# Performance work log

Hardware: AMD Instinct MI355X
Metric: run time of the kernel (lower is better)

Reference implementation:

```python
import jax, jax.numpy as jnp
import numpy as np

B, S, F, V, E, H = 128, 256, 4, 1024, 512, 1024
SCALE = 0.05


def setup_inputs() -> dict:
    key = jax.random.key(0)
    ks = jax.random.split(key, 8)
    return {
        "x": jax.random.randint(ks[0], (B, S, F), 0, V),
        "emb": jax.random.normal(ks[1], (F, V, E), dtype=jnp.float32) * SCALE,
        "proj_w": jax.random.normal(ks[2], (E, E), dtype=jnp.float32) * SCALE,
        "proj_b": jnp.zeros((E,), dtype=jnp.float32),
        "W_ih0": jax.random.normal(ks[3], (4 * H, E), dtype=jnp.float32) * SCALE,
        "W_hh0": jax.random.normal(ks[4], (4 * H, H), dtype=jnp.float32) * SCALE,
        "b_ih0": jnp.zeros((4 * H,), dtype=jnp.float32),
        "b_hh0": jnp.zeros((4 * H,), dtype=jnp.float32),
        "W_ih1": jax.random.normal(ks[5], (4 * H, H), dtype=jnp.float32) * SCALE,
        "W_hh1": jax.random.normal(ks[6], (4 * H, H), dtype=jnp.float32) * SCALE,
        "b_ih1": jnp.zeros((4 * H,), dtype=jnp.float32),
        "b_hh1": jnp.zeros((4 * H,), dtype=jnp.float32),
    }


def _lstm_cell(x_t, h, c, W_ih, W_hh, b_ih, b_hh):
    # PyTorch gate layout: [i, f, g, o] along the 4H axis.
    gates = x_t @ W_ih.T + b_ih + h @ W_hh.T + b_hh  # [B, 4H]
    i_pre, f_pre, g_pre, o_pre = jnp.split(gates, 4, axis=-1)
    c_new = jax.nn.sigmoid(f_pre) * c + jax.nn.sigmoid(i_pre) * jnp.tanh(g_pre)
    h_new = jax.nn.sigmoid(o_pre) * jnp.tanh(c_new)
    return h_new, c_new


def reference(x, emb, proj_w, proj_b,
              W_ih0, W_hh0, b_ih0, b_hh0,
              W_ih1, W_hh1, b_ih1, b_hh1):
    # Sum of per-feature embedding lookups: emb[f][x[:, :, f]]  -> [B, S, E]
    emb_sum = jnp.sum(
        jax.vmap(lambda table, idx: table[idx], in_axes=(0, 2))(emb, x), axis=0
    )
    x_in = emb_sum @ proj_w.T + proj_b  # input_proj (Linear)
    xs = jnp.swapaxes(x_in, 0, 1)  # [S, B, E] for scan over time

    z = jnp.zeros((x.shape[0], H), dtype=x_in.dtype)

    def step(carry, x_t):
        h0, c0, h1, c1 = carry
        h0, c0 = _lstm_cell(x_t, h0, c0, W_ih0, W_hh0, b_ih0, b_hh0)
        h1, c1 = _lstm_cell(h0, h1, c1, W_ih1, W_hh1, b_ih1, b_hh1)
        return (h0, c0, h1, c1), h1

    _, h1_seq = jax.lax.scan(step, (z, z, z, z), xs)  # [S, B, H]
    return jnp.swapaxes(h1_seq, 0, 1)  # [B, S, H]
```

## Files before the change

### kernel.cpp

```cpp
#include <hip/hip_runtime.h>
#include <hip/hip_bf16.h>

#define Bb    128
#define Ss    256
#define Ff    4
#define Vv    1024
#define Ee    512
#define Hh    1024
#define FourH 4096
#define Mrows (Bb * Ss)
#define NBLK  192
#define NGRP  8
#define GSZ   (NBLK / NGRP)

typedef _Float16 f16;
typedef __attribute__((ext_vector_type(8))) _Float16 half8;
typedef __attribute__((ext_vector_type(4))) float f32x4;

__global__ void cvt_f16_kernel(const float* __restrict__ s, f16* __restrict__ d, int n) {
    int i = blockIdx.x * blockDim.x + threadIdx.x;
    int stride = gridDim.x * blockDim.x;
    for (; i < n; i += stride) d[i] = (f16)s[i];
}

__global__ void bias_combine_kernel(const float* __restrict__ a, const float* __restrict__ b,
                                    const float* __restrict__ c, const float* __restrict__ d,
                                    float* __restrict__ o0, float* __restrict__ o1) {
    int i = blockIdx.x * blockDim.x + threadIdx.x;
    if (i < FourH) o0[i] = a[i] + b[i];
    else if (i < 2 * FourH) { int j = i - FourH; o1[j] = c[j] + d[j]; }
}

__global__ void emb_kernel(const int* __restrict__ x, const float* __restrict__ emb,
                           f16* __restrict__ out) {
    int r = blockIdx.x;
    int t = threadIdx.x;
    int b = r / Ss, s = r % Ss;
    const int* xr = x + (size_t)r * Ff;
    const float* e0 = emb + (size_t)xr[0] * Ee;
    const float* e1 = emb + (size_t)(Vv + xr[1]) * Ee;
    const float* e2 = emb + (size_t)(2 * Vv + xr[2]) * Ee;
    const float* e3 = emb + (size_t)(3 * Vv + xr[3]) * Ee;
    f16* orow = out + (size_t)(s * Bb + b) * Ee;
    for (int e = t; e < Ee; e += 256) orow[e] = (f16)(e0[e] + e1[e] + e2[e] + e3[e]);
}

#define BM 128
#define BN 128
#define BK 32
#define LDP 40

__global__ __launch_bounds__(256) void gemm_bt_kernel(
    const f16* __restrict__ A, const f16* __restrict__ Bw,
    const float* __restrict__ bias, f16* __restrict__ C,
    int M, int N, int K)
{
    __shared__ f16 As[BM * LDP];
    __shared__ f16 Bs[BN * LDP];
    int tid  = threadIdx.x;
    int n0   = blockIdx.x * BN;
    int m0   = blockIdx.y * BM;
    int w    = tid >> 6, lane = tid & 63;
    int wm   = (w >> 1) * 64, wn = (w & 1) * 64;
    int lrow = lane & 15, koff = lane >> 4;

    f32x4 acc[4][4] = {};

    for (int kb = 0; kb < K; kb += BK) {
        __syncthreads();
        #pragma unroll
        for (int h = 0; h < 2; ++h) {
            int ch  = tid + h * 256;
            int row = ch >> 2;
            int cc  = (ch & 3) * 8;
            *reinterpret_cast<uint4*>(&As[row * LDP + cc]) =
                *reinterpret_cast<const uint4*>(A + (size_t)(m0 + row) * K + kb + cc);
            *reinterpret_cast<uint4*>(&Bs[row * LDP + cc]) =
                *reinterpret_cast<const uint4*>(Bw + (size_t)(n0 + row) * K + kb + cc);
        }
        __syncthreads();
        half8 af[4], bf[4];
        #pragma unroll
        for (int mt = 0; mt < 4; ++mt)
            af[mt] = *reinterpret_cast<const half8*>(&As[(wm + mt * 16 + lrow) * LDP + koff * 8]);
        #pragma unroll
        for (int nt = 0; nt < 4; ++nt)
            bf[nt] = *reinterpret_cast<const half8*>(&Bs[(wn + nt * 16 + lrow) * LDP + koff * 8]);
        #pragma unroll
        for (int mt = 0; mt < 4; ++mt)
            #pragma unroll
            for (int nt = 0; nt < 4; ++nt)
                acc[mt][nt] = __builtin_amdgcn_mfma_f32_16x16x32_f16(af[mt], bf[nt], acc[mt][nt], 0, 0, 0);
    }

    #pragma unroll
    for (int mt = 0; mt < 4; ++mt)
        #pragma unroll
        for (int nt = 0; nt < 4; ++nt) {
            int col = n0 + wn + nt * 16 + lrow;
            float bv = bias[col];
            #pragma unroll
            for (int r = 0; r < 4; ++r) {
                int rowg = m0 + wm + mt * 16 + koff * 4 + r;
                C[(size_t)rowg * N + col] = (f16)(acc[mt][nt][r] + bv);
            }
        }
}

__device__ __forceinline__ void gload_lds16(const void* g, void* l) {
    __builtin_amdgcn_global_load_lds((const __attribute__((address_space(1))) void*)g,
                                     (__attribute__((address_space(3))) void*)l, 16, 0, 0);
}

__device__ __forceinline__ void gst_cc(void* p, unsigned v) {
    asm volatile("global_store_dword %0, %1, off sc0 sc1" :: "v"(p), "v"(v) : "memory");
}

__device__ __forceinline__ float f16lo(unsigned u) {
    return (float)__builtin_bit_cast(f16, (unsigned short)(u & 0xffffu));
}
__device__ __forceinline__ float f16hi(unsigned u) {
    return (float)__builtin_bit_cast(f16, (unsigned short)(u >> 16));
}

__device__ __forceinline__ unsigned aload(unsigned* p) {
    return __hip_atomic_load(p, __ATOMIC_RELAXED, __HIP_MEMORY_SCOPE_AGENT);
}

__device__ __forceinline__ void grid_sync(unsigned* bar, int wg) {
    asm volatile("s_waitcnt vmcnt(0)" ::: "memory");
    __syncthreads();
    if (threadIdx.x == 0) {
        const int g = wg & (NGRP - 1);
        unsigned* arr = bar + g * 32;
        unsigned* rel = bar + (8 + g) * 32;
        unsigned a   = atomicAdd(arr, 1u);
        unsigned gen = a / (unsigned)GSZ;
        if (a % (unsigned)GSZ == (unsigned)(GSZ - 1)) {
            const unsigned tgt = (gen + 1u) * (unsigned)GSZ;
            for (;;) {
                unsigned v0 = aload(bar + 0 * 32), v1 = aload(bar + 1 * 32);
                unsigned v2 = aload(bar + 2 * 32), v3 = aload(bar + 3 * 32);
                unsigned v4 = aload(bar + 4 * 32), v5 = aload(bar + 5 * 32);
                unsigned v6 = aload(bar + 6 * 32), v7 = aload(bar + 7 * 32);
                unsigned mn = min(min(min(v0, v1), min(v2, v3)),
                                  min(min(v4, v5), min(v6, v7)));
                if (mn >= tgt) break;
                __builtin_amdgcn_s_sleep(2);
            }
            atomicAdd(rel, 1u);
        }
        while (aload(rel) < gen + 1u) __builtin_amdgcn_s_sleep(2);
        __builtin_amdgcn_fence(__ATOMIC_ACQUIRE, "agent");
    }
    __syncthreads();
}

__device__ __forceinline__ float sigm(float v) { return 1.f / (1.f + __expf(-v)); }

__global__ __launch_bounds__(512, 2) __attribute__((amdgpu_waves_per_eu(2, 2)))
void scan_kernel(
    const f16* __restrict__ gx0,
    int t_begin, int t_end,
    const f16* __restrict__ wih1, const f16* __restrict__ whh0,
    const f16* __restrict__ whh1, const float* __restrict__ bias1,
    f16* __restrict__ h0a, f16* __restrict__ h0b,
    f16* __restrict__ h1a, f16* __restrict__ h1b,
    float* __restrict__ c0, float* __restrict__ c1,
    float* __restrict__ out, unsigned* __restrict__ bar)
{
    __shared__ __align__(1024) char smem[131072];
    float* ep = (float*)smem;

    const int tid  = threadIdx.x;
    const int wg   = blockIdx.x;
    const int lane = tid & 63;
    const int w    = tid >> 6;
    const int lrow = lane & 15, koff = lane >> 4;
    const unsigned swz   = (unsigned)((lane & 7) << 4);
    const unsigned e0s   = ((unsigned)(koff * 16)) ^ swz;
    const unsigned e1s   = ((unsigned)(64 + koff * 16)) ^ swz;
    const unsigned lane16 = (unsigned)(lane << 4);

    if (wg < 64) {
        const int rowg = wg >> 5, ug = wg & 31;
        const int np = w & 3, kh = w >> 2;
        const int u0 = ug * 32;
        const size_t growb = (size_t)rowg * 64;
        const int cw = np * 32 + lrow;

        half8 wreg[16][2];
        #pragma unroll
        for (int kc = 0; kc < 16; ++kc)
            #pragma unroll
            for (int nt = 0; nt < 2; ++nt) {
                int c = cw + nt * 16;
                wreg[kc][nt] = *(const half8*)(whh0
                    + (size_t)((c >> 5) * Hh + u0 + (c & 31)) * Hh
                    + kh * 512 + kc * 32 + koff * 8);
            }

        float creg[2][2];
        #pragma unroll
        for (int q = 0; q < 2; ++q) {
            int p = tid + q * 512, row = p >> 4, up = p & 15;
            float2 cc = *(const float2*)&c0[(growb + row) * Hh + u0 + 2 * up];
            creg[q][0] = cc.x; creg[q][1] = cc.y;
        }

        for (int i = t_begin; i < t_end; ++i) {
            if (i < 256) {
                const f16* hp = (i & 1) ? h0a : h0b;
                f16*       hw = (i & 1) ? h0b : h0a;
                const f16* gx = gx0 + (size_t)(i - t_begin) * (Bb * FourH);
                const char* hb = (const char*)hp + growb * 2048;

                unsigned gxu[2][4];
                #pragma unroll
                for (int q = 0; q < 2; ++q) {
                    int p = tid + q * 512, row = p >> 4, up = p & 15;
                    const unsigned* gr = (const unsigned*)(gx + (growb + row) * FourH + u0) + up;
                    gxu[q][0] = gr[0];
                    gxu[q][1] = gr[512];
                    gxu[q][2] = gr[1024];
                    gxu[q][3] = gr[1536];
                }

                #pragma unroll
                for (int t = 0; t < 16; ++t) {
                    int row  = w * 8 + (t >> 1);
                    int half = t & 1;
                    gload_lds16(hb + (size_t)row * 2048 + half * 1024
                                   + (lane16 ^ ((unsigned)((row & 7) << 4))),
                                smem + row * 2048 + half * 1024);
                }

                asm volatile("s_waitcnt vmcnt(0)" ::: "memory");
                __syncthreads();

                f32x4 acc[4][2] = {};
                #pragma unroll
                for (int kc = 0; kc < 16; ++kc) {
                    unsigned off = (unsigned)(kh * 1024 + (kc >> 1) * 128)
                                 + ((kc & 1) ? e1s : e0s);
                    half8 a[4];
                    #pragma unroll
                    for (int mt = 0; mt < 4; ++mt)
                        a[mt] = *(const half8*)(smem + (mt * 16 + lrow) * 2048 + off);
                    #pragma unroll
                    for (int mt = 0; mt < 4; ++mt) {
                        acc[mt][0] = __builtin_amdgcn_mfma_f32_16x16x32_f16(a[mt], wreg[kc][0], acc[mt][0], 0, 0, 0);
                        acc[mt][1] = __builtin_amdgcn_mfma_f32_16x16x32_f16(a[mt], wreg[kc][1], acc[mt][1], 0, 0, 0);
                    }
                }
                __syncthreads();
                #pragma unroll
                for (int mt = 0; mt < 4; ++mt)
                    #pragma unroll
                    for (int nt = 0; nt < 2; ++nt) {
                        int c = cw + nt * 16;
                        int rowb = mt * 16 + koff * 4;
                        #pragma unroll
                        for (int r = 0; r < 4; ++r)
                            ep[(kh * 64 + rowb + r) * 128 + c] = acc[mt][nt][r];
                    }
                __syncthreads();
                #pragma unroll
                for (int q = 0; q < 2; ++q) {
                    int p = tid + q * 512, row = p >> 4, up = p & 15, uu = 2 * up;
                    float2 iP = *(const float2*)&ep[row * 128 + uu];
                    float2 iQ = *(const float2*)&ep[(64 + row) * 128 + uu];
                    float2 fP = *(const float2*)&ep[row * 128 + 32 + uu];
                    float2 fQ = *(const float2*)&ep[(64 + row) * 128 + 32 + uu];
                    float2 gP = *(const float2*)&ep[row * 128 + 64 + uu];
                    float2 gQ = *(const float2*)&ep[(64 + row) * 128 + 64 + uu];
                    float2 oP = *(const float2*)&ep[row * 128 + 96 + uu];
                    float2 oQ = *(const float2*)&ep[(64 + row) * 128 + 96 + uu];
                    float ip0 = iP.x + iQ.x + f16lo(gxu[q][0]);
                    float ip1 = iP.y + iQ.y + f16hi(gxu[q][0]);
                    float fp0 = fP.x + fQ.x + f16lo(gxu[q][1]);
                    float fp1 = fP.y + fQ.y + f16hi(gxu[q][1]);
                    float gp0 = gP.x + gQ.x + f16lo(gxu[q][2]);
                    float gp1 = gP.y + gQ.y + f16hi(gxu[q][2]);
                    float op0 = oP.x + oQ.x + f16lo(gxu[q][3]);
                    float op1 = oP.y + oQ.y + f16hi(gxu[q][3]);
                    float cn0 = sigm(fp0) * creg[q][0] + sigm(ip0) * tanhf(gp0);
                    float cn1 = sigm(fp1) * creg[q][1] + sigm(ip1) * tanhf(gp1);
                    creg[q][0] = cn0; creg[q][1] = cn1;
                    f16 hA = (f16)(sigm(op0) * tanhf(cn0));
                    f16 hB = (f16)(sigm(op1) * tanhf(cn1));
                    unsigned hv = (unsigned)__builtin_bit_cast(unsigned short, hA)
                                | ((unsigned)__builtin_bit_cast(unsigned short, hB) << 16);
                    gst_cc((void*)(hw + (growb + row) * Hh + u0 + uu), hv);
                }
            }
            grid_sync(bar, wg);
        }
        #pragma unroll
        for (int q = 0; q < 2; ++q) {
            int p = tid + q * 512, row = p >> 4, up = p & 15;
            *(float2*)&c0[(growb + row) * Hh + u0 + 2 * up] = make_float2(creg[q][0], creg[q][1]);
        }
    } else {
        const int wgl = wg - 64;
        const int rowg = wgl >> 6, ug = wgl & 63;
        const int kq = w;
        const int u0 = ug * 16;
        const size_t growb = (size_t)rowg * 64;
        const int l7 = lane & 7;

        const f16* wbase = (kq < 4) ? wih1 : whh1;
        half8 wreg[8][4];
        #pragma unroll
        for (int kc = 0; kc < 8; ++kc)
            #pragma unroll
            for (int nt = 0; nt < 4; ++nt)
                wreg[kc][nt] = *(const half8*)(wbase
                    + (size_t)(nt * Hh + u0 + lrow) * Hh
                    + (kq & 3) * 256 + kc * 32 + koff * 8);

        const int erow = tid >> 3, eup = tid & 7, euu = 2 * eup;
        float crg0, crg1;
        { float2 cc = *(const float2*)&c1[(growb + erow) * Hh + u0 + euu];
          crg0 = cc.x; crg1 = cc.y; }
        float2 bI = *(const float2*)&bias1[u0 + euu];
        float2 bF = *(const float2*)&bias1[Hh + u0 + euu];
        float2 bG = *(const float2*)&bias1[2 * Hh + u0 + euu];
        float2 bO = *(const float2*)&bias1[3 * Hh + u0 + euu];

        const unsigned wb = (unsigned)kq * 16384u;
        const int r2 = lane >> 5;
        const int chs0 = lane & 31;

        #define STG(rb_, bo_) { \
            _Pragma("unroll") \
            for (int t = 0; t < 8; ++t) { \
                int rl = (rb_) + t * 2 + r2; \
                gload_lds16(src + (size_t)rl * 2048 \
                                + ((unsigned)((chs0 ^ (rl & 7)) << 4)), \
                            smem + wb + (bo_) + (unsigned)(t * 1024)); \
            } }
        #define CMT(mt_, bo_) { \
            _Pragma("unroll") \
            for (int kc = 0; kc < 8; ++kc) { \
                half8 a = *(const half8*)(smem + wb + (bo_) \
                            + (unsigned)(lrow * 512) \
                            + ((unsigned)(((kc * 4 + koff) ^ l7) << 4))); \
                acc[mt_][0] = __builtin_amdgcn_mfma_f32_16x16x32_f16(a, wreg[kc][0], acc[mt_][0], 0, 0, 0); \
                acc[mt_][1] = __builtin_amdgcn_mfma_f32_16x16x32_f16(a, wreg[kc][1], acc[mt_][1], 0, 0, 0); \
                acc[mt_][2] = __builtin_amdgcn_mfma_f32_16x16x32_f16(a, wreg[kc][2], acc[mt_][2], 0, 0, 0); \
                acc[mt_][3] = __builtin_amdgcn_mfma_f32_16x16x32_f16(a, wreg[kc][3], acc[mt_][3], 0, 0, 0); \
            } }

        for (int i = t_begin; i < t_end; ++i) {
            int t1 = i - 1;
            if (t1 >= 0) {
                const f16* a0 = (t1 & 1) ? h0b : h0a;
                const f16* a1 = (t1 & 1) ? h1a : h1b;
                f16*       hw = (t1 & 1) ? h1b : h1a;
                const char* src = ((kq < 4) ? (const char*)a0 : (const char*)a1)
                                + growb * 2048 + (size_t)(kq & 3) * 512;

                f32x4 acc[4][4] = {};
                STG(0, 0u)
                STG(16, 8192u)
                asm volatile("s_waitcnt vmcnt(8)" ::: "memory");
                CMT(0, 0u)
                asm volatile("s_waitcnt lgkmcnt(0)" ::: "memory");
                STG(32, 0u)
                asm volatile("s_waitcnt vmcnt(8)" ::: "memory");
                CMT(1, 8192u)
                asm volatile("s_waitcnt lgkmcnt(0)" ::: "memory");
                STG(48, 8192u)
                asm volatile("s_waitcnt vmcnt(8)" ::: "memory");
                CMT(2, 0u)
                asm volatile("s_waitcnt vmcnt(0)" ::: "memory");
                CMT(3, 8192u)

                #pragma unroll
                for (int mt = 0; mt < 4; ++mt)
                    #pragma unroll
                    for (int nt = 0; nt < 4; ++nt) {
                        int c = nt * 16 + lrow;
                        #pragma unroll
                        for (int r = 0; r < 4; ++r) {
                            int row = mt * 16 + koff * 4 + r;
                            int sw  = (row ^ (row >> 2)) & 3;
                            *(float*)(smem + wb + (unsigned)(row * 256)
                                      + (unsigned)((c ^ (sw << 4)) * 4)) = acc[mt][nt][r];
                        }
                    }
                __syncthreads();
                {
                    int sw = (erow ^ (erow >> 2)) & 3;
                    const char* rbase = smem + (unsigned)(erow * 256);
                    float s0x = bI.x, s0y = bI.y, s1x = bF.x, s1y = bF.y;
                    float s2x = bG.x, s2y = bG.y, s3x = bO.x, s3y = bO.y;
                    #pragma unroll
                    for (int k8 = 0; k8 < 8; ++k8) {
                        const char* base = rbase + (unsigned)k8 * 16384u;
                        float2 v0 = *(const float2*)(base + (unsigned)((( 0 + euu) ^ (sw << 4)) * 4));
                        float2 v1 = *(const float2*)(base + (unsigned)(((16 + euu) ^ (sw << 4)) * 4));
                        float2 v2 = *(const float2*)(base + (unsigned)(((32 + euu) ^ (sw << 4)) * 4));
                        float2 v3 = *(const float2*)(base + (unsigned)(((48 + euu) ^ (sw << 4)) * 4));
                        s0x += v0.x; s0y += v0.y; s1x += v1.x; s1y += v1.y;
                        s2x += v2.x; s2y += v2.y; s3x += v3.x; s3y += v3.y;
                    }
                    float cn0 = sigm(s1x) * crg0 + sigm(s0x) * tanhf(s2x); crg0 = cn0;
                    float cn1 = sigm(s1y) * crg1 + sigm(s0y) * tanhf(s2y); crg1 = cn1;
                    float hn0 = sigm(s3x) * tanhf(cn0);
                    float hn1 = sigm(s3y) * tanhf(cn1);
                    unsigned hv = (unsigned)__builtin_bit_cast(unsigned short, (f16)hn0)
                                | ((unsigned)__builtin_bit_cast(unsigned short, (f16)hn1) << 16);
                    gst_cc((void*)(hw + (growb + erow) * Hh + u0 + euu), hv);
                    *(float2*)&out[(growb + erow) * (size_t)(Ss * Hh)
                                   + (size_t)t1 * Hh + u0 + euu] = make_float2(hn0, hn1);
                }
            }
            grid_sync(bar, wg);
        }
        *(float2*)&c1[(growb + erow) * Hh + u0 + euu] = make_float2(crg0, crg1);
        #undef STG
        #undef CMT
    }
}

extern "C" void kernel_launch(void* const* d_in, const int* in_sizes, int n_in,
                              void* d_out, int out_size, void* d_ws, size_t ws_size,
                              hipStream_t stream) {
    const int*   x      = (const int*)  d_in[0];
    const float* emb    = (const float*)d_in[1];
    const float* proj_w = (const float*)d_in[2];
    const float* proj_b = (const float*)d_in[3];
    const float* W_ih0  = (const float*)d_in[4];
    const float* W_hh0  = (const float*)d_in[5];
    const float* b_ih0  = (const float*)d_in[6];
    const float* b_hh0  = (const float*)d_in[7];
    const float* W_ih1  = (const float*)d_in[8];
    const float* W_hh1  = (const float*)d_in[9];
    const float* b_ih1  = (const float*)d_in[10];
    const float* b_hh1  = (const float*)d_in[11];
    float* out = (float*)d_out;

    char* ws = (char*)d_ws;
    f16* emb_sum = (f16*)(ws);
    f16* x_in    = (f16*)(ws + 33554432ull);
    f16* gates   = (f16*)(ws + 67108864ull);
    char* wp     = ws + 201326592ull;
    f16* pw_f   = (f16*)wp; wp += (size_t)Ee * Ee * 2;
    f16* wih0_f = (f16*)wp; wp += (size_t)FourH * Ee * 2;
    f16* whh0_f = (f16*)wp; wp += (size_t)FourH * Hh * 2;
    f16* wih1_f = (f16*)wp; wp += (size_t)FourH * Hh * 2;
    f16* whh1_f = (f16*)wp; wp += (size_t)FourH * Hh * 2;
    float* bias0 = (float*)wp; wp += FourH * 4;
    float* bias1 = (float*)wp; wp += FourH * 4;
    char* zbase = wp;
    f16*   h0a = (f16*)wp;   wp += (size_t)Bb * Hh * 2;
    f16*   h0b = (f16*)wp;   wp += (size_t)Bb * Hh * 2;
    f16*   h1a = (f16*)wp;   wp += (size_t)Bb * Hh * 2;
    f16*   h1b = (f16*)wp;   wp += (size_t)Bb * Hh * 2;
    float* c0  = (float*)wp; wp += (size_t)Bb * Hh * 4;
    float* c1  = (float*)wp; wp += (size_t)Bb * Hh * 4;
    unsigned* bar = (unsigned*)wp; wp += 4096;
    size_t zbytes = (size_t)(wp - zbase);

    cvt_f16_kernel<<<512, 256, 0, stream>>>(proj_w, pw_f,   Ee * Ee);
    cvt_f16_kernel<<<512, 256, 0, stream>>>(W_ih0,  wih0_f, FourH * Ee);
    cvt_f16_kernel<<<512, 256, 0, stream>>>(W_hh0,  whh0_f, FourH * Hh);
    cvt_f16_kernel<<<512, 256, 0, stream>>>(W_ih1,  wih1_f, FourH * Hh);
    cvt_f16_kernel<<<512, 256, 0, stream>>>(W_hh1,  whh1_f, FourH * Hh);
    bias_combine_kernel<<<32, 256, 0, stream>>>(b_ih0, b_hh0, b_ih1, b_hh1, bias0, bias1);
    hipMemsetAsync(zbase, 0, zbytes, stream);

    emb_kernel<<<Mrows, 256, 0, stream>>>(x, emb, emb_sum);
    gemm_bt_kernel<<<dim3(Ee / BN, Mrows / BM), 256, 0, stream>>>(
        emb_sum, pw_f, proj_b, x_in, Mrows, Ee, Ee);

    const int CM = Mrows / 2;

    for (int half = 0; half < 2; ++half) {
        gemm_bt_kernel<<<dim3(FourH / BN, CM / BM), 256, 0, stream>>>(
            x_in + (size_t)half * CM * Ee, wih0_f, bias0, gates, CM, FourH, Ee);
        int tb = half * 128;
        int te = (half == 0) ? 128 : 257;
        const f16* gxp = gates;
        void* args[] = { (void*)&gxp, (void*)&tb, (void*)&te,
                         (void*)&wih1_f, (void*)&whh0_f, (void*)&whh1_f, (void*)&bias1,
                         (void*)&h0a, (void*)&h0b, (void*)&h1a, (void*)&h1b,
                         (void*)&c0, (void*)&c1, (void*)&out, (void*)&bar };
        hipLaunchCooperativeKernel((const void*)scan_kernel, dim3(NBLK), dim3(512),
                                   args, 0, stream);
    }
}
```

Before: 3.119 ms.

## Replace global grid barrier with per-layer group barriers and h0 ring buffer

Removes the full-grid barrier between timesteps. Layer-0 and layer-1 workgroups now each sync only within their own row-group counters, with point-to-point waits where they depend on each other. The layer-0 hidden state becomes a 4-slot ring buffer, so layer 0 can run up to two steps ahead of layer 1 without overwriting state layer 1 still needs. This is meant to cut barrier latency and let the two layers pipeline. The cost is more complex sync logic, with a risk of ordering bugs: the layer-1 wait has no acquire fence, and the barrier counters carry across the two launches.

```diff
diff --git a/kernel.cpp b/kernel.cpp
--- a/kernel.cpp
+++ b/kernel.cpp
@@ -10,8 +10,6 @@
 #define FourH 4096
 #define Mrows (Bb * Ss)
 #define NBLK  192
-#define NGRP  8
-#define GSZ   (NBLK / NGRP)
 
 typedef _Float16 f16;
 typedef __attribute__((ext_vector_type(8))) _Float16 half8;
@@ -127,35 +125,6 @@
     return __hip_atomic_load(p, __ATOMIC_RELAXED, __HIP_MEMORY_SCOPE_AGENT);
 }
 
-__device__ __forceinline__ void grid_sync(unsigned* bar, int wg) {
-    asm volatile("s_waitcnt vmcnt(0)" ::: "memory");
-    __syncthreads();
-    if (threadIdx.x == 0) {
-        const int g = wg & (NGRP - 1);
-        unsigned* arr = bar + g * 32;
-        unsigned* rel = bar + (8 + g) * 32;
-        unsigned a   = atomicAdd(arr, 1u);
-        unsigned gen = a / (unsigned)GSZ;
-        if (a % (unsigned)GSZ == (unsigned)(GSZ - 1)) {
-            const unsigned tgt = (gen + 1u) * (unsigned)GSZ;
-            for (;;) {
-                unsigned v0 = aload(bar + 0 * 32), v1 = aload(bar + 1 * 32);
-                unsigned v2 = aload(bar + 2 * 32), v3 = aload(bar + 3 * 32);
-                unsigned v4 = aload(bar + 4 * 32), v5 = aload(bar + 5 * 32);
-                unsigned v6 = aload(bar + 6 * 32), v7 = aload(bar + 7 * 32);
-                unsigned mn = min(min(min(v0, v1), min(v2, v3)),
-                                  min(min(v4, v5), min(v6, v7)));
-                if (mn >= tgt) break;
-                __builtin_amdgcn_s_sleep(2);
-            }
-            atomicAdd(rel, 1u);
-        }
-        while (aload(rel) < gen + 1u) __builtin_amdgcn_s_sleep(2);
-        __builtin_amdgcn_fence(__ATOMIC_ACQUIRE, "agent");
-    }
-    __syncthreads();
-}
-
 __device__ __forceinline__ float sigm(float v) { return 1.f / (1.f + __expf(-v)); }
 
 __global__ __launch_bounds__(512, 2) __attribute__((amdgpu_waves_per_eu(2, 2)))
@@ -164,7 +133,7 @@
     int t_begin, int t_end,
     const f16* __restrict__ wih1, const f16* __restrict__ whh0,
     const f16* __restrict__ whh1, const float* __restrict__ bias1,
-    f16* __restrict__ h0a, f16* __restrict__ h0b,
+    f16* __restrict__ h0r,
     f16* __restrict__ h1a, f16* __restrict__ h1b,
     float* __restrict__ c0, float* __restrict__ c1,
     float* __restrict__ out, unsigned* __restrict__ bar)
@@ -181,6 +150,7 @@
     const unsigned e0s   = ((unsigned)(koff * 16)) ^ swz;
     const unsigned e1s   = ((unsigned)(64 + koff * 16)) ^ swz;
     const unsigned lane16 = (unsigned)(lane << 4);
+    const size_t HSLOT = (size_t)Bb * Hh;
 
     if (wg < 64) {
         const int rowg = wg >> 5, ug = wg & 31;
@@ -188,6 +158,10 @@
         const int u0 = ug * 32;
         const size_t growb = (size_t)rowg * 64;
         const int cw = np * 32 + lrow;
+
+        unsigned* arr0 = bar + (0 + rowg) * 32;
+        unsigned* rel0 = bar + (2 + rowg) * 32;
+        unsigned* rel1 = bar + (6 + rowg) * 32;
 
         half8 wreg[16][2];
         #pragma unroll
@@ -210,8 +184,8 @@
 
         for (int i = t_begin; i < t_end; ++i) {
             if (i < 256) {
-                const f16* hp = (i & 1) ? h0a : h0b;
-                f16*       hw = (i & 1) ? h0b : h0a;
+                const f16* hp = h0r + (size_t)((unsigned)((i - 1) & 3)) * HSLOT;
+                f16*       hw = h0r + (size_t)(i & 3) * HSLOT;
                 const f16* gx = gx0 + (size_t)(i - t_begin) * (Bb * FourH);
                 const char* hb = (const char*)hp + growb * 2048;
 
@@ -264,6 +238,9 @@
                         for (int r = 0; r < 4; ++r)
                             ep[(kh * 64 + rowb + r) * 128 + c] = acc[mt][nt][r];
                     }
+                if (tid == 0) {
+                    while ((int)aload(rel1) < i - 2) __builtin_amdgcn_s_sleep(2);
+                }
                 __syncthreads();
                 #pragma unroll
                 for (int q = 0; q < 2; ++q) {
@@ -294,7 +271,16 @@
                     gst_cc((void*)(hw + (growb + row) * Hh + u0 + uu), hv);
                 }
             }
-            grid_sync(bar, wg);
+            asm volatile("s_waitcnt vmcnt(0)" ::: "memory");
+            __syncthreads();
+            if (tid == 0) {
+                unsigned a = atomicAdd(arr0, 1u);
+                unsigned gen = a >> 5;
+                if ((a & 31u) == 31u) atomicAdd(rel0, 1u);
+                while (aload(rel0) < gen + 1u) __builtin_amdgcn_s_sleep(2);
+                __builtin_amdgcn_fence(__ATOMIC_ACQUIRE, "agent");
+            }
+            __syncthreads();
         }
         #pragma unroll
         for (int q = 0; q < 2; ++q) {
@@ -308,6 +294,10 @@
         const int u0 = ug * 16;
         const size_t growb = (size_t)rowg * 64;
         const int l7 = lane & 7;
+
+        unsigned* arr1 = bar + (4 + rowg) * 32;
+        unsigned* rel1 = bar + (6 + rowg) * 32;
+        unsigned* rel0 = bar + (2 + rowg) * 32;
 
         const f16* wbase = (kq < 4) ? wih1 : whh1;
         half8 wreg[8][4];
@@ -355,7 +345,13 @@
         for (int i = t_begin; i < t_end; ++i) {
             int t1 = i - 1;
             if (t1 >= 0) {
-                const f16* a0 = (t1 & 1) ? h0b : h0a;
+                if (tid == 0) {
+                    while ((int)aload(rel0) < i) __builtin_amdgcn_s_sleep(2);
+                    __builtin_amdgcn_fence(__ATOMIC_ACQUIRE, "agent");
+                }
+                __syncthreads();
+
+                const f16* a0 = h0r + (size_t)(t1 & 3) * HSLOT;
                 const f16* a1 = (t1 & 1) ? h1a : h1b;
                 f16*       hw = (t1 & 1) ? h1b : h1a;
                 const char* src = ((kq < 4) ? (const char*)a0 : (const char*)a1)
@@ -417,7 +413,15 @@
                                    + (size_t)t1 * Hh + u0 + euu] = make_float2(hn0, hn1);
                 }
             }
-            grid_sync(bar, wg);
+            asm volatile("s_waitcnt vmcnt(0)" ::: "memory");
+            __syncthreads();
+            if (tid == 0) {
+                unsigned a = atomicAdd(arr1, 1u);
+                unsigned gen = a >> 6;
+                if ((a & 63u) == 63u) atomicAdd(rel1, 1u);
+                while (aload(rel1) < gen + 1u) __builtin_amdgcn_s_sleep(2);
+            }
+            __syncthreads();
         }
         *(float2*)&c1[(growb + erow) * Hh + u0 + euu] = make_float2(crg0, crg1);
         #undef STG
@@ -455,8 +459,7 @@
     float* bias0 = (float*)wp; wp += FourH * 4;
     float* bias1 = (float*)wp; wp += FourH * 4;
     char* zbase = wp;
-    f16*   h0a = (f16*)wp;   wp += (size_t)Bb * Hh * 2;
-    f16*   h0b = (f16*)wp;   wp += (size_t)Bb * Hh * 2;
+    f16*   h0r = (f16*)wp;   wp += 4ull * Bb * Hh * 2;
     f16*   h1a = (f16*)wp;   wp += (size_t)Bb * Hh * 2;
     f16*   h1b = (f16*)wp;   wp += (size_t)Bb * Hh * 2;
     float* c0  = (float*)wp; wp += (size_t)Bb * Hh * 4;
@@ -486,7 +489,7 @@
         const f16* gxp = gates;
         void* args[] = { (void*)&gxp, (void*)&tb, (void*)&te,
                          (void*)&wih1_f, (void*)&whh0_f, (void*)&whh1_f, (void*)&bias1,
-                         (void*)&h0a, (void*)&h0b, (void*)&h1a, (void*)&h1b,
+                         (void*)&h0r, (void*)&h1a, (void*)&h1b,
                          (void*)&c0, (void*)&c1, (void*)&out, (void*)&bar };
         hipLaunchCooperativeKernel((const void*)scan_kernel, dim3(NBLK), dim3(512),
                                    args, 0, stream);
```

Result: faster. 2.998 ms (-3.9%).
